# Optimization experiments

Hardware: AMD Instinct MI355X
Metric: run time of the kernel (lower is better)

## Reference

```python
import jax, jax.numpy as jnp
import numpy as np

B, T, C = 4, 4096, 1024
DEGREE, EXPAND = 2, 2
H = EXPAND * C  # selector / inner dim = 2048


def setup_inputs() -> dict:
    key = jax.random.key(0)
    ks = jax.random.split(key, 4)
    sc = lambda d: 1.0 / np.sqrt(d)
    return {
        "x": jax.random.normal(ks[0], (B, T, C), jnp.float32),
        "W_sel": jax.random.normal(ks[1], (C, H), jnp.float32) * sc(C),
        "W_agg": jax.random.normal(ks[2], (C, DEGREE * H), jnp.float32) * sc(C),
        "W_out": jax.random.normal(ks[3], (H, C), jnp.float32) * sc(H),
        "sqk_q": jnp.ones((H,), jnp.float32),
        "sqk_k": jnp.ones((DEGREE * H,), jnp.float32),
    }


def reference(x, W_sel, W_agg, W_out, sqk_q, sqk_k):
    # Selector branch on queries (gated): B,T,H
    s = jax.nn.silu(jnp.einsum('btc,ch->bth', x, W_sel) * sqk_q)
    # Aggregator branch on context: B,T,DEGREE*H
    h = jnp.einsum('btc,cd->btd', x, W_agg) * sqk_k
    chunks = jnp.split(h, DEGREE, axis=-1)
    # Polynomial expansion: sum_{d=1..DEGREE} prod_{k<=d} chunk_k  -> B,T,H
    p = chunks[0]
    poly = p
    for c in chunks[1:]:
        p = p * c
        poly = poly + p
    # Causal masked mean: tril(ones(T,T)) @ poly / row-count == cumsum / arange.
    # Honors the causal structure without materializing the T x T mask.
    denom = jnp.arange(1, T + 1, dtype=poly.dtype)[None, :, None]
    agg = jnp.cumsum(poly, axis=1) / denom  # B,T,H causal running mean
    # Mix selected queries with aggregated polynomial state, project out.
    return jnp.einsum('bth,hc->btc', s * agg, W_out)
```

## Files before the change

### kernel.cpp

```cpp
#include <hip/hip_runtime.h>
#include <hip/hip_bf16.h>
#include <stdint.h>

#define BB 4
#define TT 4096
#define CC 1024
#define HH 2048
#define MM (BB*TT)
#define NCK 32
#define CKS 128

using short8 = __attribute__((ext_vector_type(8))) short;
using f32x4  = __attribute__((ext_vector_type(4))) float;

__device__ __forceinline__ unsigned short f2bf(float f) {
    union { float f; uint32_t u; } v; v.f = f;
    uint32_t r = v.u + 0x7fffu + ((v.u >> 16) & 1u);
    return (unsigned short)(r >> 16);
}
__device__ __forceinline__ float bf_lo(uint32_t u) {
    union { uint32_t u; float f; } v; v.u = u << 16; return v.f;
}
__device__ __forceinline__ float bf_hi(uint32_t u) {
    union { uint32_t u; float f; } v; v.u = u & 0xFFFF0000u; return v.f;
}
__device__ __forceinline__ uint32_t pack2bf(float lo, float hi) {
    return ((uint32_t)f2bf(lo)) | (((uint32_t)f2bf(hi)) << 16);
}

__global__ void conv_x_kernel(const float* __restrict__ x, unsigned short* __restrict__ xb, int n4) {
    int i = blockIdx.x * blockDim.x + threadIdx.x;
    if (i >= n4) return;
    float4 v = ((const float4*)x)[i];
    ushort4 o;
    o.x = f2bf(v.x); o.y = f2bf(v.y); o.z = f2bf(v.z); o.w = f2bf(v.w);
    ((ushort4*)xb)[i] = o;
}

__global__ void trans_direct_kernel(const float* __restrict__ in, unsigned short* __restrict__ out,
                                    const float* __restrict__ scale, int R, int Cin) {
    __shared__ float tile[32][33];
    int c0 = blockIdx.x * 32, k0 = blockIdx.y * 32;
    int tx = threadIdx.x;
    for (int i = threadIdx.y; i < 32; i += 8) {
        float s = scale ? scale[c0 + tx] : 1.f;
        tile[i][tx] = in[(size_t)(k0 + i) * Cin + c0 + tx] * s;
    }
    __syncthreads();
    for (int i = threadIdx.y; i < 32; i += 8)
        out[(size_t)(c0 + i) * R + k0 + tx] = f2bf(tile[tx][i]);
}

__global__ void trans_pair_kernel(const float* __restrict__ in, unsigned short* __restrict__ out,
                                  const float* __restrict__ scale) {
    __shared__ float tile[32][33];
    int q0 = blockIdx.x * 32, k0 = blockIdx.y * 32;
    int g = q0 >> 5;
    int tx = threadIdx.x;
    int c = (tx < 16) ? (g * 16 + tx) : (2048 + g * 16 + tx - 16);
    float s = scale[c];
    for (int i = threadIdx.y; i < 32; i += 8)
        tile[i][tx] = in[(size_t)(k0 + i) * 4096 + c] * s;
    __syncthreads();
    for (int i = threadIdx.y; i < 32; i += 8)
        out[(size_t)(q0 + i) * 1024 + k0 + tx] = f2bf(tile[tx][i]);
}

template<int LDK, int NT>
__device__ __forceinline__ void gemm_core(
    const unsigned short* __restrict__ A,
    const unsigned short* __restrict__ Bt,
    int m0, int n0, int tid,
    f32x4 (&acc)[8][4])
{
    __shared__ __align__(16) unsigned short As[4 * 8192];
    __shared__ __align__(16) unsigned short Bs[4 * 8192];

    const int lane = tid & 63;
    const int wave = tid >> 6;
    const int l15  = lane & 15;
    const int quad = lane >> 4;
    const int wm = (wave >> 2) << 7;
    const int wn = (wave & 3) << 6;

#pragma unroll
    for (int i = 0; i < 8; i++)
#pragma unroll
        for (int j = 0; j < 4; j++) acc[i][j] = {0.f, 0.f, 0.f, 0.f};

    const int rl  = tid >> 2;
    const int kc8 = ((tid & 3) ^ ((tid >> 3) & 3)) << 3;
    const unsigned short* gA = A  + (size_t)(m0 + rl) * LDK + kc8;
    const unsigned short* gB = Bt + (size_t)(n0 + rl) * LDK + kc8;

#define STAGE(G, L) __builtin_amdgcn_global_load_lds( \
        (const __attribute__((address_space(1))) void*)(G), \
        (__attribute__((address_space(3))) void*)(L), 16, 0, 0)
#define SWZ(row) ((quad ^ (((row) >> 1) & 3)) << 3)

#pragma unroll
    for (int t = 0; t < 2; t++) {
        STAGE(gA + t * 32,                     &As[t * 8192 + tid * 8]);
        STAGE(gA + 128 * (size_t)LDK + t * 32, &As[t * 8192 + 4096 + tid * 8]);
        STAGE(gB + t * 32,                     &Bs[t * 8192 + tid * 8]);
        STAGE(gB + 128 * (size_t)LDK + t * 32, &Bs[t * 8192 + 4096 + tid * 8]);
    }
    asm volatile("s_waitcnt vmcnt(4)" ::: "memory");
    __builtin_amdgcn_s_barrier();

    for (int t = 0; t < NT; ++t) {
        const unsigned short* as = &As[(t & 3) * 8192];
        const unsigned short* bs = &Bs[(t & 3) * 8192];
        unsigned short* asd = &As[((t + 2) & 3) * 8192];
        unsigned short* bsd = &Bs[((t + 2) & 3) * 8192];
        const bool pf = (t + 2) < NT;

        short8 af[4], bf[4];
#pragma unroll
        for (int i = 0; i < 4; i++) {
            int row = wm + i * 16 + l15;
            af[i] = *(const short8*)(as + row * 32 + SWZ(row));
        }
#pragma unroll
        for (int j = 0; j < 4; j++) {
            int row = wn + j * 16 + l15;
            bf[j] = *(const short8*)(bs + row * 32 + SWZ(row));
        }
        if (pf) {
            STAGE(gA + (size_t)(t + 2) * 32,                     asd + tid * 8);
            STAGE(gA + 128 * (size_t)LDK + (size_t)(t + 2) * 32, asd + 4096 + tid * 8);
        }
        __builtin_amdgcn_s_barrier();
        asm volatile("s_waitcnt lgkmcnt(0)" ::: "memory");
        __builtin_amdgcn_sched_barrier(0);
        __builtin_amdgcn_s_setprio(1);
#pragma unroll
        for (int i = 0; i < 4; i++)
#pragma unroll
            for (int j = 0; j < 4; j++)
                acc[i][j] = __builtin_amdgcn_mfma_f32_16x16x32_bf16(af[i], bf[j], acc[i][j], 0, 0, 0);
        __builtin_amdgcn_s_setprio(0);
        __builtin_amdgcn_sched_barrier(0);
        __builtin_amdgcn_s_barrier();

        short8 ag[4];
#pragma unroll
        for (int i = 0; i < 4; i++) {
            int row = wm + 64 + i * 16 + l15;
            ag[i] = *(const short8*)(as + row * 32 + SWZ(row));
        }
        if (pf) {
            STAGE(gB + (size_t)(t + 2) * 32,                     bsd + tid * 8);
            STAGE(gB + 128 * (size_t)LDK + (size_t)(t + 2) * 32, bsd + 4096 + tid * 8);
        }
        __builtin_amdgcn_s_barrier();
        asm volatile("s_waitcnt lgkmcnt(0)" ::: "memory");
        __builtin_amdgcn_sched_barrier(0);
        __builtin_amdgcn_s_setprio(1);
#pragma unroll
        for (int i = 0; i < 4; i++)
#pragma unroll
            for (int j = 0; j < 4; j++)
                acc[4 + i][j] = __builtin_amdgcn_mfma_f32_16x16x32_bf16(ag[i], bf[j], acc[4 + i][j], 0, 0, 0);
        __builtin_amdgcn_s_setprio(0);
        __builtin_amdgcn_sched_barrier(0);
        if (t < NT - 2) { asm volatile("s_waitcnt vmcnt(4)" ::: "memory"); }
        else            { asm volatile("s_waitcnt vmcnt(0)" ::: "memory"); }
        __builtin_amdgcn_s_barrier();
    }
#undef STAGE
#undef SWZ
}

__global__ __launch_bounds__(512, 2) void gemm_fused_kernel(
    const unsigned short* __restrict__ A,
    const unsigned short* __restrict__ Bt,
    unsigned short* __restrict__ Sout,
    unsigned short* __restrict__ Pout,
    float* __restrict__ part)
{
    __shared__ float psum[256];
    const int tid = threadIdx.x;
    const int xcd = blockIdx.x & 7;
    const int j   = blockIdx.x >> 3;
    const int mt  = j / 3;
    const int nt  = xcd * 3 + (j % 3);
    const int m0 = mt << 8, n0 = nt << 8;
    if (tid < 256) psum[tid] = 0.f;

    f32x4 acc[8][4];
    gemm_core<1024, 32>(A, Bt, m0, n0, tid, acc);

    const int lane = tid & 63;
    const int wave = tid >> 6;
    const int l15  = lane & 15;
    const int quad = lane >> 4;
    const int wm = (wave >> 2) << 7;
    const int wn = (wave & 3) << 6;

    if (nt < 8) {
#pragma unroll
        for (int i = 0; i < 8; i++)
#pragma unroll
            for (int j2 = 0; j2 < 4; j2++) {
                int col = n0 + wn + j2 * 16 + l15;
#pragma unroll
                for (int r = 0; r < 4; r++) {
                    int row = m0 + wm + i * 16 + quad * 4 + r;
                    float v = acc[i][j2][r];
                    v = v / (1.f + __expf(-v));
                    Sout[(size_t)row * 2048 + col] = f2bf(v);
                }
            }
    } else {
        const int pbase = ((n0 - 2048 + wn) >> 1);
        float lsum0 = 0.f, lsum1 = 0.f;
#pragma unroll
        for (int i = 0; i < 8; i++) {
#pragma unroll
            for (int jp = 0; jp < 2; jp++) {
                int pcol = pbase + jp * 16 + l15;
#pragma unroll
                for (int r = 0; r < 4; r++) {
                    int row = m0 + wm + i * 16 + quad * 4 + r;
                    float pv = acc[i][2 * jp][r] * (1.f + acc[i][2 * jp + 1][r]);
                    Pout[(size_t)row * 2048 + pcol] = f2bf(pv);
                    if (jp == 0) lsum0 += pv; else lsum1 += pv;
                }
            }
        }
        int base = (wm >> 7) * 128 + (wn >> 1) + l15;
        atomicAdd(&psum[base], lsum0);
        atomicAdd(&psum[base + 16], lsum1);
        __syncthreads();
        if (tid < 256) {
            int b  = m0 >> 12;
            int ck = ((m0 & 4095) >> 7) + (tid >> 7);
            part[((size_t)b * NCK + ck) * 2048 + ((n0 - 2048) >> 1) + (tid & 127)] = psum[tid];
        }
    }
}

__global__ __launch_bounds__(512, 2) void gemm_out_kernel(
    const unsigned short* __restrict__ A,
    const unsigned short* __restrict__ Bt,
    float* __restrict__ Cout)
{
    const int tid = threadIdx.x;
    const int nt  = blockIdx.x & 3;
    const int mt  = (blockIdx.x >> 3) + 32 * ((blockIdx.x >> 2) & 1);
    const int m0 = mt << 8, n0 = nt << 8;

    f32x4 acc[8][4];
    gemm_core<2048, 64>(A, Bt, m0, n0, tid, acc);

    const int lane = tid & 63;
    const int wave = tid >> 6;
    const int l15  = lane & 15;
    const int quad = lane >> 4;
    const int wm = (wave >> 2) << 7;
    const int wn = (wave & 3) << 6;
#pragma unroll
    for (int i = 0; i < 8; i++)
#pragma unroll
        for (int j = 0; j < 4; j++) {
            int col = n0 + wn + j * 16 + l15;
#pragma unroll
            for (int r = 0; r < 4; r++) {
                int row = m0 + wm + i * 16 + quad * 4 + r;
                Cout[(size_t)row * 1024 + col] = acc[i][j][r];
            }
        }
}

__global__ void chunk_scan_kernel(float* __restrict__ part) {
    int idx = blockIdx.x * blockDim.x + threadIdx.x;
    int b = idx >> 11, col = idx & 2047;
    float run = 0.f;
    for (int ck = 0; ck < NCK; ck++) {
        size_t off = ((size_t)b * NCK + ck) * 2048 + col;
        float v = part[off];
        part[off] = run;
        run += v;
    }
}

__global__ void finalize_kernel(unsigned short* __restrict__ poly, const unsigned short* __restrict__ s,
                                const float* __restrict__ part) {
    int seg = blockIdx.x & 3;
    int ck  = (blockIdx.x >> 2) & (NCK - 1);
    int b   = blockIdx.x >> 7;
    int cp  = seg * 256 + threadIdx.x;
    size_t po = ((size_t)b * NCK + ck) * 2048 + cp * 2;
    float run0 = part[po], run1 = part[po + 1];
    size_t base = ((size_t)b * TT + (size_t)ck * CKS) * 2048 + cp * 2;
    for (int t = 0; t < CKS; t++) {
        int tg = ck * CKS + t;
        size_t off = base + (size_t)t * 2048;
        uint32_t pv = *(const uint32_t*)&poly[off];
        run0 += bf_lo(pv);
        run1 += bf_hi(pv);
        float inv = 1.f / (float)(tg + 1);
        uint32_t sv = *(const uint32_t*)&s[off];
        float m0 = bf_lo(sv) * run0 * inv;
        float m1 = bf_hi(sv) * run1 * inv;
        *(uint32_t*)&poly[off] = pack2bf(m0, m1);
    }
}

extern "C" void kernel_launch(void* const* d_in, const int* in_sizes, int n_in,
                              void* d_out, int out_size, void* d_ws, size_t ws_size,
                              hipStream_t stream) {
    const float* x     = (const float*)d_in[0];
    const float* W_sel = (const float*)d_in[1];
    const float* W_agg = (const float*)d_in[2];
    const float* W_out = (const float*)d_in[3];
    const float* sqk_q = (const float*)d_in[4];
    const float* sqk_k = (const float*)d_in[5];
    float* out = (float*)d_out;

    char* ws = (char*)d_ws;
    unsigned short* xb    = (unsigned short*)(ws);
    unsigned short* wallT = (unsigned short*)(ws + 33554432ull);
    unsigned short* woutT = (unsigned short*)(ws + 46137344ull);
    unsigned short* s_b   = (unsigned short*)(ws + 50331648ull);
    unsigned short* poly  = (unsigned short*)(ws + 117440512ull);
    float*          part  = (float*)(ws + 184549376ull);

    dim3 tb(32, 8);
    conv_x_kernel<<<(MM * CC / 4 + 255) / 256, 256, 0, stream>>>(x, xb, MM * CC / 4);
    trans_direct_kernel<<<dim3(HH / 32, CC / 32), tb, 0, stream>>>(W_sel, wallT, sqk_q, CC, HH);
    trans_pair_kernel<<<dim3(4096 / 32, CC / 32), tb, 0, stream>>>(W_agg, wallT + 2048ull * 1024, sqk_k);
    trans_direct_kernel<<<dim3(CC / 32, HH / 32), tb, 0, stream>>>(W_out, woutT, nullptr, HH, CC);

    gemm_fused_kernel<<<(MM / 256) * 24, 512, 0, stream>>>(xb, wallT, s_b, poly, part);

    chunk_scan_kernel<<<(BB * HH) / 256, 256, 0, stream>>>(part);
    finalize_kernel<<<BB * NCK * 4, 256, 0, stream>>>(poly, s_b, part);

    gemm_out_kernel<<<(MM / 256) * (CC / 256), 512, 0, stream>>>(poly, woutT, out);
}
```

Before: 484.1 us.

## Shrink GEMM block tile to 128x256 with 4 waves and triple-buffered LDS

Changes both GEMM kernels from 512-thread blocks computing 256x256 tiles to 256-thread blocks computing 128x256 tiles. Each wave now covers all 128 rows and a 64-column slice. The LDS ring drops from four buffers to three rotating buffers (current, next, staging), with the vmcnt thresholds adjusted. Block-to-XCD mapping for the output GEMM is also reworked. The goal is more blocks and less LDS per block for better occupancy and load balance, at the cost of lower B-tile reuse per block and more global traffic for the weight operand.

```diff
diff --git a/kernel.cpp b/kernel.cpp
--- a/kernel.cpp
+++ b/kernel.cpp
@@ -73,15 +73,13 @@
     int m0, int n0, int tid,
     f32x4 (&acc)[8][4])
 {
-    __shared__ __align__(16) unsigned short As[4 * 8192];
-    __shared__ __align__(16) unsigned short Bs[4 * 8192];
+    __shared__ __align__(16) unsigned short As[3 * 4096];
+    __shared__ __align__(16) unsigned short Bs[3 * 8192];
 
     const int lane = tid & 63;
-    const int wave = tid >> 6;
     const int l15  = lane & 15;
     const int quad = lane >> 4;
-    const int wm = (wave >> 2) << 7;
-    const int wn = (wave & 3) << 6;
+    const int wn   = (tid >> 6) << 6;
 
 #pragma unroll
     for (int i = 0; i < 8; i++)
@@ -100,35 +98,36 @@
 
 #pragma unroll
     for (int t = 0; t < 2; t++) {
-        STAGE(gA + t * 32,                     &As[t * 8192 + tid * 8]);
-        STAGE(gA + 128 * (size_t)LDK + t * 32, &As[t * 8192 + 4096 + tid * 8]);
-        STAGE(gB + t * 32,                     &Bs[t * 8192 + tid * 8]);
-        STAGE(gB + 128 * (size_t)LDK + t * 32, &Bs[t * 8192 + 4096 + tid * 8]);
-    }
-    asm volatile("s_waitcnt vmcnt(4)" ::: "memory");
+        STAGE(gA + t * 32,                    &As[t * 4096 + tid * 8]);
+        STAGE(gA + 64 * (size_t)LDK + t * 32, &As[t * 4096 + 2048 + tid * 8]);
+#pragma unroll
+        for (int u = 0; u < 4; u++)
+            STAGE(gB + (size_t)(u * 64) * LDK + t * 32, &Bs[t * 8192 + u * 2048 + tid * 8]);
+    }
+    asm volatile("s_waitcnt vmcnt(6)" ::: "memory");
     __builtin_amdgcn_s_barrier();
 
+    unsigned short* aC = As;            unsigned short* bC = Bs;
+    unsigned short* aN = As + 4096;     unsigned short* bN = Bs + 8192;
+    unsigned short* aS = As + 8192;     unsigned short* bS = Bs + 16384;
+
     for (int t = 0; t < NT; ++t) {
-        const unsigned short* as = &As[(t & 3) * 8192];
-        const unsigned short* bs = &Bs[(t & 3) * 8192];
-        unsigned short* asd = &As[((t + 2) & 3) * 8192];
-        unsigned short* bsd = &Bs[((t + 2) & 3) * 8192];
         const bool pf = (t + 2) < NT;
 
         short8 af[4], bf[4];
 #pragma unroll
         for (int i = 0; i < 4; i++) {
-            int row = wm + i * 16 + l15;
-            af[i] = *(const short8*)(as + row * 32 + SWZ(row));
+            int row = i * 16 + l15;
+            af[i] = *(const short8*)(aC + row * 32 + SWZ(row));
         }
 #pragma unroll
         for (int j = 0; j < 4; j++) {
             int row = wn + j * 16 + l15;
-            bf[j] = *(const short8*)(bs + row * 32 + SWZ(row));
+            bf[j] = *(const short8*)(bC + row * 32 + SWZ(row));
         }
         if (pf) {
-            STAGE(gA + (size_t)(t + 2) * 32,                     asd + tid * 8);
-            STAGE(gA + 128 * (size_t)LDK + (size_t)(t + 2) * 32, asd + 4096 + tid * 8);
+            STAGE(gA + (size_t)(t + 2) * 32,                    aS + tid * 8);
+            STAGE(gA + 64 * (size_t)LDK + (size_t)(t + 2) * 32, aS + 2048 + tid * 8);
         }
         __builtin_amdgcn_s_barrier();
         asm volatile("s_waitcnt lgkmcnt(0)" ::: "memory");
@@ -146,12 +145,13 @@
         short8 ag[4];
 #pragma unroll
         for (int i = 0; i < 4; i++) {
-            int row = wm + 64 + i * 16 + l15;
-            ag[i] = *(const short8*)(as + row * 32 + SWZ(row));
+            int row = 64 + i * 16 + l15;
+            ag[i] = *(const short8*)(aC + row * 32 + SWZ(row));
         }
         if (pf) {
-            STAGE(gB + (size_t)(t + 2) * 32,                     bsd + tid * 8);
-            STAGE(gB + 128 * (size_t)LDK + (size_t)(t + 2) * 32, bsd + 4096 + tid * 8);
+#pragma unroll
+            for (int u = 0; u < 4; u++)
+                STAGE(gB + (size_t)(u * 64) * LDK + (size_t)(t + 2) * 32, bS + u * 2048 + tid * 8);
         }
         __builtin_amdgcn_s_barrier();
         asm volatile("s_waitcnt lgkmcnt(0)" ::: "memory");
@@ -164,39 +164,40 @@
                 acc[4 + i][j] = __builtin_amdgcn_mfma_f32_16x16x32_bf16(ag[i], bf[j], acc[4 + i][j], 0, 0, 0);
         __builtin_amdgcn_s_setprio(0);
         __builtin_amdgcn_sched_barrier(0);
-        if (t < NT - 2) { asm volatile("s_waitcnt vmcnt(4)" ::: "memory"); }
+        if (t < NT - 2) { asm volatile("s_waitcnt vmcnt(6)" ::: "memory"); }
         else            { asm volatile("s_waitcnt vmcnt(0)" ::: "memory"); }
         __builtin_amdgcn_s_barrier();
+
+        unsigned short* ta = aC; aC = aN; aN = aS; aS = ta;
+        unsigned short* tb = bC; bC = bN; bN = bS; bS = tb;
     }
 #undef STAGE
 #undef SWZ
 }
 
-__global__ __launch_bounds__(512, 2) void gemm_fused_kernel(
+__global__ __launch_bounds__(256, 2) void gemm_fused_kernel(
     const unsigned short* __restrict__ A,
     const unsigned short* __restrict__ Bt,
     unsigned short* __restrict__ Sout,
     unsigned short* __restrict__ Pout,
     float* __restrict__ part)
 {
-    __shared__ float psum[256];
+    __shared__ float psum[128];
     const int tid = threadIdx.x;
     const int xcd = blockIdx.x & 7;
     const int j   = blockIdx.x >> 3;
     const int mt  = j / 3;
     const int nt  = xcd * 3 + (j % 3);
-    const int m0 = mt << 8, n0 = nt << 8;
-    if (tid < 256) psum[tid] = 0.f;
+    const int m0 = mt << 7, n0 = nt << 8;
+    if (tid < 128) psum[tid] = 0.f;
 
     f32x4 acc[8][4];
     gemm_core<1024, 32>(A, Bt, m0, n0, tid, acc);
 
     const int lane = tid & 63;
-    const int wave = tid >> 6;
     const int l15  = lane & 15;
     const int quad = lane >> 4;
-    const int wm = (wave >> 2) << 7;
-    const int wn = (wave & 3) << 6;
+    const int wn   = (tid >> 6) << 6;
 
     if (nt < 8) {
 #pragma unroll
@@ -206,7 +207,7 @@
                 int col = n0 + wn + j2 * 16 + l15;
 #pragma unroll
                 for (int r = 0; r < 4; r++) {
-                    int row = m0 + wm + i * 16 + quad * 4 + r;
+                    int row = m0 + i * 16 + quad * 4 + r;
                     float v = acc[i][j2][r];
                     v = v / (1.f + __expf(-v));
                     Sout[(size_t)row * 2048 + col] = f2bf(v);
@@ -222,53 +223,53 @@
                 int pcol = pbase + jp * 16 + l15;
 #pragma unroll
                 for (int r = 0; r < 4; r++) {
-                    int row = m0 + wm + i * 16 + quad * 4 + r;
+                    int row = m0 + i * 16 + quad * 4 + r;
                     float pv = acc[i][2 * jp][r] * (1.f + acc[i][2 * jp + 1][r]);
                     Pout[(size_t)row * 2048 + pcol] = f2bf(pv);
                     if (jp == 0) lsum0 += pv; else lsum1 += pv;
                 }
             }
         }
-        int base = (wm >> 7) * 128 + (wn >> 1) + l15;
+        int base = (wn >> 1) + l15;
         atomicAdd(&psum[base], lsum0);
         atomicAdd(&psum[base + 16], lsum1);
         __syncthreads();
-        if (tid < 256) {
+        if (tid < 128) {
             int b  = m0 >> 12;
-            int ck = ((m0 & 4095) >> 7) + (tid >> 7);
-            part[((size_t)b * NCK + ck) * 2048 + ((n0 - 2048) >> 1) + (tid & 127)] = psum[tid];
-        }
-    }
-}
-
-__global__ __launch_bounds__(512, 2) void gemm_out_kernel(
+            int ck = (m0 & 4095) >> 7;
+            part[((size_t)b * NCK + ck) * 2048 + ((n0 - 2048) >> 1) + tid] = psum[tid];
+        }
+    }
+}
+
+__global__ __launch_bounds__(256, 2) void gemm_out_kernel(
     const unsigned short* __restrict__ A,
     const unsigned short* __restrict__ Bt,
     float* __restrict__ Cout)
 {
     const int tid = threadIdx.x;
-    const int nt  = blockIdx.x & 3;
-    const int mt  = (blockIdx.x >> 3) + 32 * ((blockIdx.x >> 2) & 1);
-    const int m0 = mt << 8, n0 = nt << 8;
+    const int xcd = blockIdx.x & 7;
+    const int j   = blockIdx.x >> 3;
+    const int nt  = xcd >> 1;
+    const int mt  = (xcd & 1) * 64 + j;
+    const int m0 = mt << 7, n0 = nt << 8;
 
     f32x4 acc[8][4];
     gemm_core<2048, 64>(A, Bt, m0, n0, tid, acc);
 
     const int lane = tid & 63;
-    const int wave = tid >> 6;
     const int l15  = lane & 15;
     const int quad = lane >> 4;
-    const int wm = (wave >> 2) << 7;
-    const int wn = (wave & 3) << 6;
+    const int wn   = (tid >> 6) << 6;
 #pragma unroll
     for (int i = 0; i < 8; i++)
 #pragma unroll
-        for (int j = 0; j < 4; j++) {
-            int col = n0 + wn + j * 16 + l15;
+        for (int j2 = 0; j2 < 4; j2++) {
+            int col = n0 + wn + j2 * 16 + l15;
 #pragma unroll
             for (int r = 0; r < 4; r++) {
-                int row = m0 + wm + i * 16 + quad * 4 + r;
-                Cout[(size_t)row * 1024 + col] = acc[i][j][r];
+                int row = m0 + i * 16 + quad * 4 + r;
+                Cout[(size_t)row * 1024 + col] = acc[i][j2][r];
             }
         }
 }
@@ -333,10 +334,10 @@
     trans_pair_kernel<<<dim3(4096 / 32, CC / 32), tb, 0, stream>>>(W_agg, wallT + 2048ull * 1024, sqk_k);
     trans_direct_kernel<<<dim3(CC / 32, HH / 32), tb, 0, stream>>>(W_out, woutT, nullptr, HH, CC);
 
-    gemm_fused_kernel<<<(MM / 256) * 24, 512, 0, stream>>>(xb, wallT, s_b, poly, part);
+    gemm_fused_kernel<<<(MM / 128) * 24, 256, 0, stream>>>(xb, wallT, s_b, poly, part);
 
     chunk_scan_kernel<<<(BB * HH) / 256, 256, 0, stream>>>(part);
     finalize_kernel<<<BB * NCK * 4, 256, 0, stream>>>(poly, s_b, part);
 
-    gemm_out_kernel<<<(MM / 256) * (CC / 256), 512, 0, stream>>>(poly, woutT, out);
-}
+    gemm_out_kernel<<<(MM / 128) * (CC / 256), 256, 0, stream>>>(poly, woutT, out);
+}
```

Result: no change. 482.3 us (-0.4%).
